# Performance work log

Hardware: AMD Instinct MI355X
Metric: run time of the kernel (lower is better)

Reference implementation:

```python
import jax, jax.numpy as jnp
import numpy as np

BASE_SPARSITY = 0.15


def setup_inputs() -> dict:
    key = jax.random.key(0)
    k1, k2 = jax.random.split(key)
    B, F, D, H = 8, 4096, 1024, 8
    x_freq = jax.random.normal(k1, (B, F, D), dtype=jnp.float32)
    W_imp = jax.random.normal(k2, (D, H), dtype=jnp.float32) / np.sqrt(D)
    b_imp = jnp.zeros((H,), dtype=jnp.float32)
    sparsity_offset = jnp.zeros((H,), dtype=jnp.float32)
    return {"x_freq": x_freq, "W_imp": W_imp, "b_imp": b_imp,
            "sparsity_offset": sparsity_offset}


def reference(x_freq, W_imp, b_imp, sparsity_offset):
    B, F, D = x_freq.shape
    H = W_imp.shape[1]
    head_dim = D // H

    # per-head k is derived through Python int() in the original -> trace-time constant
    off_np = np.asarray(sparsity_offset, dtype=np.float64)
    sparsity_np = 1.0 / (1.0 + np.exp(-off_np)) * 0.3 + BASE_SPARSITY
    ks = [max(1, int(F * sparsity_np[h])) for h in range(H)]

    magnitude = jnp.abs(x_freq)                                  # (B,F,D)
    scores = jnp.einsum('bfd,dh->bfh', magnitude, W_imp) + b_imp  # (B,F,H)

    batch_idx = jnp.arange(B)[:, None]
    masks = []
    for h in range(H):
        _, topk_idx = jax.lax.top_k(scores[:, :, h], ks[h])       # (B,k)
        mask_h = jnp.zeros((B, F), dtype=x_freq.dtype).at[batch_idx, topk_idx].set(1.0)
        masks.append(mask_h)
    mask = jnp.stack(masks, axis=-1)                              # (B,F,H)

    x_filtered = (x_freq.reshape(B, F, H, head_dim) * mask[..., None]).reshape(B, F, D)
    return x_filtered, mask
```

## Files before the change

kernel.cpp:

```cpp
#include <hip/hip_runtime.h>
#include <math.h>

#define BB 8
#define FF 4096
#define DD 1024
#define HH 8
#define BF (BB * FF)

__global__ __launch_bounds__(256) void k_scores(const float* __restrict__ x,
                                                const float* __restrict__ W,
                                                const float* __restrict__ b,
                                                float* __restrict__ scoresT) {
    const int lane = threadIdx.x & 63;
    const int wid  = blockIdx.x * 4 + (threadIdx.x >> 6);
    const int r0   = wid * 4;

    double acc[4][8];
#pragma unroll
    for (int r = 0; r < 4; ++r)
#pragma unroll
        for (int h = 0; h < 8; ++h) acc[r][h] = 0.0;

#pragma unroll
    for (int j = 0; j < 4; ++j) {
        const int dbase = (lane + 64 * j) * 4;
        float wv[4][8];
#pragma unroll
        for (int c = 0; c < 4; ++c) {
            const float4* wp = (const float4*)(W + (size_t)(dbase + c) * HH);
            float4 w0 = wp[0], w1 = wp[1];
            wv[c][0] = w0.x; wv[c][1] = w0.y; wv[c][2] = w0.z; wv[c][3] = w0.w;
            wv[c][4] = w1.x; wv[c][5] = w1.y; wv[c][6] = w1.z; wv[c][7] = w1.w;
        }
#pragma unroll
        for (int r = 0; r < 4; ++r) {
            float4 v = ((const float4*)(x + (size_t)(r0 + r) * DD))[lane + 64 * j];
            const float m0 = fabsf(v.x), m1 = fabsf(v.y),
                        m2 = fabsf(v.z), m3 = fabsf(v.w);
#pragma unroll
            for (int h = 0; h < 8; ++h)
                acc[r][h] += (double)m0 * (double)wv[0][h]
                           + (double)m1 * (double)wv[1][h]
                           + (double)m2 * (double)wv[2][h]
                           + (double)m3 * (double)wv[3][h];
        }
    }

    const int b5 = (lane >> 5) & 1, b4 = (lane >> 4) & 1, b3 = (lane >> 3) & 1;
#pragma unroll
    for (int r = 0; r < 4; ++r) {
        double t[4];
#pragma unroll
        for (int i = 0; i < 4; ++i) {
            double send = b5 ? acc[r][i] : acc[r][4 + i];
            double recv = __shfl_xor(send, 32, 64);
            t[i] = (b5 ? acc[r][4 + i] : acc[r][i]) + recv;
        }
        double u[2];
#pragma unroll
        for (int i = 0; i < 2; ++i) {
            double send = b4 ? t[i] : t[2 + i];
            double recv = __shfl_xor(send, 16, 64);
            u[i] = (b4 ? t[2 + i] : t[i]) + recv;
        }
        double s;
        {
            double send = b3 ? u[0] : u[1];
            double recv = __shfl_xor(send, 8, 64);
            s = (b3 ? u[1] : u[0]) + recv;
        }
        s += __shfl_xor(s, 4, 64);
        s += __shfl_xor(s, 2, 64);
        s += __shfl_xor(s, 1, 64);
        if ((lane & 7) == 0) {
            const int h = lane >> 3;
            scoresT[(size_t)h * BF + (r0 + r)] = (float)(s + (double)b[h]);
        }
    }
}

__global__ __launch_bounds__(256) void k_topk(float* scoresT,
                                              const float* __restrict__ soff) {
    const int blk = blockIdx.x;
    const int b   = blk >> 3;
    const int h   = blk & 7;
    const int tid = threadIdx.x;

    __shared__ unsigned int keys[FF];
    __shared__ unsigned int hist[256];
    __shared__ unsigned int scan[256];
    __shared__ unsigned int sh_digit, sh_rem;

    double o  = (double)soff[h];
    double sp = 1.0 / (1.0 + exp(-o)) * 0.3 + 0.15;
    int k = (int)((double)FF * sp);
    if (k < 1) k = 1;

    const size_t base = (size_t)h * BF + (size_t)b * FF;

    for (int i = 0; i < 16; ++i) {
        const int f = i * 256 + tid;
        const unsigned int u = __float_as_uint(scoresT[base + f]);
        keys[f] = (u & 0x80000000u) ? ~u : (u | 0x80000000u);
    }
    __syncthreads();

    unsigned int remaining = (unsigned int)k;
    unsigned int prefix = 0, pmask = 0;
    for (int pass = 3; pass >= 0; --pass) {
        const int shift = pass * 8;
        hist[tid] = 0;
        __syncthreads();
        for (int i = 0; i < 16; ++i) {
            const unsigned int key = keys[i * 256 + tid];
            if ((key & pmask) == prefix)
                atomicAdd(&hist[(key >> shift) & 255u], 1u);
        }
        __syncthreads();
        scan[tid] = hist[tid];
        for (int off = 1; off < 256; off <<= 1) {
            __syncthreads();
            const unsigned int add = (tid + off < 256) ? scan[tid + off] : 0u;
            __syncthreads();
            scan[tid] += add;
        }
        __syncthreads();
        const unsigned int Sd    = scan[tid];
        const unsigned int Snext = (tid < 255) ? scan[tid + 1] : 0u;
        if (Sd >= remaining && Snext < remaining) {
            sh_digit = (unsigned int)tid;
            sh_rem   = remaining - Snext;
        }
        __syncthreads();
        prefix |= sh_digit << shift;
        pmask  |= 255u << shift;
        remaining = sh_rem;
        __syncthreads();
    }

    unsigned int cnt = 0;
    for (int i = 0; i < 16; ++i) cnt += (keys[tid * 16 + i] == prefix);
    scan[tid] = cnt;
    for (int off = 1; off < 256; off <<= 1) {
        __syncthreads();
        const unsigned int add = (tid >= off) ? scan[tid - off] : 0u;
        __syncthreads();
        scan[tid] += add;
    }
    __syncthreads();
    unsigned int rank = scan[tid] - cnt;

    float mbuf[16];
    for (int i = 0; i < 16; ++i) {
        const unsigned int key = keys[tid * 16 + i];
        float m = 0.0f;
        if (key > prefix) {
            m = 1.0f;
        } else if (key == prefix) {
            m = (rank < remaining) ? 1.0f : 0.0f;
            rank++;
        }
        mbuf[i] = m;
    }
    float4* dst = (float4*)(scoresT + base + (size_t)tid * 16);
    for (int q = 0; q < 4; ++q)
        dst[q] = make_float4(mbuf[q * 4], mbuf[q * 4 + 1], mbuf[q * 4 + 2], mbuf[q * 4 + 3]);
}

__global__ __launch_bounds__(256) void k_filter(const float* __restrict__ x,
                                                const float* __restrict__ maskT,
                                                float* __restrict__ out_x,
                                                float* __restrict__ out_mask) {
    const size_t total4 = (size_t)BB * FF * DD / 4;
    const size_t stride = (size_t)gridDim.x * blockDim.x;
    const float4* x4 = (const float4*)x;
    float4* o4 = (float4*)out_x;
    for (size_t i = (size_t)blockIdx.x * blockDim.x + threadIdx.x;
         i < total4; i += stride) {
        const size_t r = i >> 8;
        const unsigned int j = (unsigned int)i & 255u;
        const unsigned int h = j >> 5;
        const float mv = maskT[(size_t)h * BF + r];
        float4 v = x4[i];
        v.x *= mv; v.y *= mv; v.z *= mv; v.w *= mv;
        o4[i] = v;
        if (j < 8)
            out_mask[r * HH + j] = maskT[(size_t)j * BF + r];
    }
}

extern "C" void kernel_launch(void* const* d_in, const int* in_sizes, int n_in,
                              void* d_out, int out_size, void* d_ws, size_t ws_size,
                              hipStream_t stream) {
    const float* x  = (const float*)d_in[0];
    const float* W  = (const float*)d_in[1];
    const float* bi = (const float*)d_in[2];
    const float* so = (const float*)d_in[3];

    float* out_x    = (float*)d_out;
    float* out_mask = (float*)d_out + (size_t)BB * FF * DD;
    float* scoresT  = (float*)d_ws;

    k_scores<<<2048, 256, 0, stream>>>(x, W, bi, scoresT);
    k_topk<<<BB * HH, 256, 0, stream>>>(scoresT, so);
    k_filter<<<8192, 256, 0, stream>>>(x, scoresT, out_x, out_mask);
}
```

Before: 302.4 us.

## Restructure scores to one row per wave, use wave-shuffle scans in top-k, skip masked loads

The scores kernel now assigns one row per wavefront instead of four, with all x loads issued up front. It uses launch bounds for higher occupancy and four times as many blocks, at the cost of reloading W per row. Top-k replaces the shared-memory Hillis-Steele scans with wave-level shuffle scans and uses per-wave histograms to reduce atomic contention and barrier count. The filter kernel unrolls a fixed four iterations and skips reading x where the mask is zero, cutting read traffic for the roughly 70% of masked-out head slices. The masked path writes zeros instead of x times zero, so NaN or Inf inputs would now come out as 0 rather than NaN.

```diff
diff --git a/kernel.cpp b/kernel.cpp
--- a/kernel.cpp
+++ b/kernel.cpp
@@ -7,22 +7,26 @@
 #define HH 8
 #define BF (BB * FF)
 
-__global__ __launch_bounds__(256) void k_scores(const float* __restrict__ x,
-                                                const float* __restrict__ W,
-                                                const float* __restrict__ b,
-                                                float* __restrict__ scoresT) {
+__global__ __launch_bounds__(256, 4) void k_scores(const float* __restrict__ x,
+                                                   const float* __restrict__ W,
+                                                   const float* __restrict__ b,
+                                                   float* __restrict__ scoresT) {
     const int lane = threadIdx.x & 63;
-    const int wid  = blockIdx.x * 4 + (threadIdx.x >> 6);
-    const int r0   = wid * 4;
-
-    double acc[4][8];
-#pragma unroll
-    for (int r = 0; r < 4; ++r)
-#pragma unroll
-        for (int h = 0; h < 8; ++h) acc[r][h] = 0.0;
+    const int r    = (int)((blockIdx.x * blockDim.x + threadIdx.x) >> 6);
+
+    const float4* px = (const float4*)(x + (size_t)r * DD);
+    float4 xv0 = px[lane];
+    float4 xv1 = px[lane + 64];
+    float4 xv2 = px[lane + 128];
+    float4 xv3 = px[lane + 192];
+
+    double acc[8];
+#pragma unroll
+    for (int h = 0; h < 8; ++h) acc[h] = 0.0;
 
 #pragma unroll
     for (int j = 0; j < 4; ++j) {
+        __builtin_amdgcn_sched_barrier(0);
         const int dbase = (lane + 64 * j) * 4;
         float wv[4][8];
 #pragma unroll
@@ -32,63 +36,59 @@
             wv[c][0] = w0.x; wv[c][1] = w0.y; wv[c][2] = w0.z; wv[c][3] = w0.w;
             wv[c][4] = w1.x; wv[c][5] = w1.y; wv[c][6] = w1.z; wv[c][7] = w1.w;
         }
-#pragma unroll
-        for (int r = 0; r < 4; ++r) {
-            float4 v = ((const float4*)(x + (size_t)(r0 + r) * DD))[lane + 64 * j];
-            const float m0 = fabsf(v.x), m1 = fabsf(v.y),
-                        m2 = fabsf(v.z), m3 = fabsf(v.w);
-#pragma unroll
-            for (int h = 0; h < 8; ++h)
-                acc[r][h] += (double)m0 * (double)wv[0][h]
-                           + (double)m1 * (double)wv[1][h]
-                           + (double)m2 * (double)wv[2][h]
-                           + (double)m3 * (double)wv[3][h];
-        }
+        const float4 v = (j == 0) ? xv0 : (j == 1) ? xv1 : (j == 2) ? xv2 : xv3;
+        const float m0 = fabsf(v.x), m1 = fabsf(v.y),
+                    m2 = fabsf(v.z), m3 = fabsf(v.w);
+#pragma unroll
+        for (int h = 0; h < 8; ++h)
+            acc[h] += (double)m0 * (double)wv[0][h]
+                    + (double)m1 * (double)wv[1][h]
+                    + (double)m2 * (double)wv[2][h]
+                    + (double)m3 * (double)wv[3][h];
     }
 
     const int b5 = (lane >> 5) & 1, b4 = (lane >> 4) & 1, b3 = (lane >> 3) & 1;
-#pragma unroll
-    for (int r = 0; r < 4; ++r) {
-        double t[4];
-#pragma unroll
-        for (int i = 0; i < 4; ++i) {
-            double send = b5 ? acc[r][i] : acc[r][4 + i];
-            double recv = __shfl_xor(send, 32, 64);
-            t[i] = (b5 ? acc[r][4 + i] : acc[r][i]) + recv;
-        }
-        double u[2];
-#pragma unroll
-        for (int i = 0; i < 2; ++i) {
-            double send = b4 ? t[i] : t[2 + i];
-            double recv = __shfl_xor(send, 16, 64);
-            u[i] = (b4 ? t[2 + i] : t[i]) + recv;
-        }
-        double s;
-        {
-            double send = b3 ? u[0] : u[1];
-            double recv = __shfl_xor(send, 8, 64);
-            s = (b3 ? u[1] : u[0]) + recv;
-        }
-        s += __shfl_xor(s, 4, 64);
-        s += __shfl_xor(s, 2, 64);
-        s += __shfl_xor(s, 1, 64);
-        if ((lane & 7) == 0) {
-            const int h = lane >> 3;
-            scoresT[(size_t)h * BF + (r0 + r)] = (float)(s + (double)b[h]);
-        }
+    double t[4];
+#pragma unroll
+    for (int i = 0; i < 4; ++i) {
+        double send = b5 ? acc[i] : acc[4 + i];
+        double recv = __shfl_xor(send, 32, 64);
+        t[i] = (b5 ? acc[4 + i] : acc[i]) + recv;
+    }
+    double u[2];
+#pragma unroll
+    for (int i = 0; i < 2; ++i) {
+        double send = b4 ? t[i] : t[2 + i];
+        double recv = __shfl_xor(send, 16, 64);
+        u[i] = (b4 ? t[2 + i] : t[i]) + recv;
+    }
+    double s;
+    {
+        double send = b3 ? u[0] : u[1];
+        double recv = __shfl_xor(send, 8, 64);
+        s = (b3 ? u[1] : u[0]) + recv;
+    }
+    s += __shfl_xor(s, 4, 64);
+    s += __shfl_xor(s, 2, 64);
+    s += __shfl_xor(s, 1, 64);
+    if ((lane & 7) == 0) {
+        const int h = lane >> 3;
+        scoresT[(size_t)h * BF + r] = (float)(s + (double)b[h]);
     }
 }
 
 __global__ __launch_bounds__(256) void k_topk(float* scoresT,
                                               const float* __restrict__ soff) {
-    const int blk = blockIdx.x;
-    const int b   = blk >> 3;
-    const int h   = blk & 7;
-    const int tid = threadIdx.x;
+    const int blk  = blockIdx.x;
+    const int b    = blk >> 3;
+    const int h    = blk & 7;
+    const int tid  = threadIdx.x;
+    const int lane = tid & 63;
+    const int w    = tid >> 6;
 
     __shared__ unsigned int keys[FF];
-    __shared__ unsigned int hist[256];
-    __shared__ unsigned int scan[256];
+    __shared__ unsigned int hist4[4][256];
+    __shared__ unsigned int wsum[4];
     __shared__ unsigned int sh_digit, sh_rem;
 
     double o  = (double)soff[h];
@@ -103,52 +103,61 @@
         const unsigned int u = __float_as_uint(scoresT[base + f]);
         keys[f] = (u & 0x80000000u) ? ~u : (u | 0x80000000u);
     }
+#pragma unroll
+    for (int q = 0; q < 4; ++q) hist4[q][tid] = 0u;
     __syncthreads();
 
     unsigned int remaining = (unsigned int)k;
     unsigned int prefix = 0, pmask = 0;
     for (int pass = 3; pass >= 0; --pass) {
         const int shift = pass * 8;
-        hist[tid] = 0;
-        __syncthreads();
         for (int i = 0; i < 16; ++i) {
             const unsigned int key = keys[i * 256 + tid];
             if ((key & pmask) == prefix)
-                atomicAdd(&hist[(key >> shift) & 255u], 1u);
+                atomicAdd(&hist4[w][(key >> shift) & 255u], 1u);
         }
         __syncthreads();
-        scan[tid] = hist[tid];
-        for (int off = 1; off < 256; off <<= 1) {
-            __syncthreads();
-            const unsigned int add = (tid + off < 256) ? scan[tid + off] : 0u;
-            __syncthreads();
-            scan[tid] += add;
-        }
+        const int rbin = 255 - tid;
+        const unsigned int c = hist4[0][rbin] + hist4[1][rbin] +
+                               hist4[2][rbin] + hist4[3][rbin];
+        unsigned int P = c;
+#pragma unroll
+        for (int o2 = 1; o2 < 64; o2 <<= 1) {
+            const unsigned int tt = __shfl_up(P, o2, 64);
+            if (lane >= o2) P += tt;
+        }
+        if (lane == 63) wsum[w] = P;
         __syncthreads();
-        const unsigned int Sd    = scan[tid];
-        const unsigned int Snext = (tid < 255) ? scan[tid + 1] : 0u;
-        if (Sd >= remaining && Snext < remaining) {
-            sh_digit = (unsigned int)tid;
-            sh_rem   = remaining - Snext;
-        }
+        unsigned int off = 0;
+#pragma unroll
+        for (int w2 = 0; w2 < 4; ++w2) if (w2 < w) off += wsum[w2];
+        P += off;
+        if (P >= remaining && (P - c) < remaining) {
+            sh_digit = (unsigned int)rbin;
+            sh_rem   = remaining - (P - c);
+        }
+#pragma unroll
+        for (int q = 0; q < 4; ++q) hist4[q][tid] = 0u;
         __syncthreads();
         prefix |= sh_digit << shift;
         pmask  |= 255u << shift;
         remaining = sh_rem;
-        __syncthreads();
     }
 
     unsigned int cnt = 0;
     for (int i = 0; i < 16; ++i) cnt += (keys[tid * 16 + i] == prefix);
-    scan[tid] = cnt;
-    for (int off = 1; off < 256; off <<= 1) {
-        __syncthreads();
-        const unsigned int add = (tid >= off) ? scan[tid - off] : 0u;
-        __syncthreads();
-        scan[tid] += add;
-    }
+    unsigned int inc = cnt;
+#pragma unroll
+    for (int o2 = 1; o2 < 64; o2 <<= 1) {
+        const unsigned int tt = __shfl_up(inc, o2, 64);
+        if (lane >= o2) inc += tt;
+    }
+    if (lane == 63) wsum[w] = inc;
     __syncthreads();
-    unsigned int rank = scan[tid] - cnt;
+    unsigned int off = 0;
+#pragma unroll
+    for (int w2 = 0; w2 < 4; ++w2) if (w2 < w) off += wsum[w2];
+    unsigned int rank = off + inc - cnt;
 
     float mbuf[16];
     for (int i = 0; i < 16; ++i) {
@@ -163,26 +172,29 @@
         mbuf[i] = m;
     }
     float4* dst = (float4*)(scoresT + base + (size_t)tid * 16);
+#pragma unroll
     for (int q = 0; q < 4; ++q)
-        dst[q] = make_float4(mbuf[q * 4], mbuf[q * 4 + 1], mbuf[q * 4 + 2], mbuf[q * 4 + 3]);
+        dst[q] = make_float4(mbuf[q * 4], mbuf[q * 4 + 1],
+                             mbuf[q * 4 + 2], mbuf[q * 4 + 3]);
 }
 
 __global__ __launch_bounds__(256) void k_filter(const float* __restrict__ x,
                                                 const float* __restrict__ maskT,
                                                 float* __restrict__ out_x,
                                                 float* __restrict__ out_mask) {
-    const size_t total4 = (size_t)BB * FF * DD / 4;
     const size_t stride = (size_t)gridDim.x * blockDim.x;
+    const size_t i0 = (size_t)blockIdx.x * blockDim.x + threadIdx.x;
     const float4* x4 = (const float4*)x;
     float4* o4 = (float4*)out_x;
-    for (size_t i = (size_t)blockIdx.x * blockDim.x + threadIdx.x;
-         i < total4; i += stride) {
+#pragma unroll
+    for (int it = 0; it < 4; ++it) {
+        const size_t i = i0 + (size_t)it * stride;
         const size_t r = i >> 8;
         const unsigned int j = (unsigned int)i & 255u;
         const unsigned int h = j >> 5;
         const float mv = maskT[(size_t)h * BF + r];
-        float4 v = x4[i];
-        v.x *= mv; v.y *= mv; v.z *= mv; v.w *= mv;
+        float4 v = make_float4(0.f, 0.f, 0.f, 0.f);
+        if (mv != 0.0f) v = x4[i];
         o4[i] = v;
         if (j < 8)
             out_mask[r * HH + j] = maskT[(size_t)j * BF + r];
@@ -201,7 +213,7 @@
     float* out_mask = (float*)d_out + (size_t)BB * FF * DD;
     float* scoresT  = (float*)d_ws;
 
-    k_scores<<<2048, 256, 0, stream>>>(x, W, bi, scoresT);
+    k_scores<<<8192, 256, 0, stream>>>(x, W, bi, scoresT);
     k_topk<<<BB * HH, 256, 0, stream>>>(scoresT, so);
     k_filter<<<8192, 256, 0, stream>>>(x, scoresT, out_x, out_mask);
 }
```

Measured after the change: 337.7 us. +11.7%, slower.
